# Kernel tuning notes

Hardware: AMD Instinct MI355X
Metric: run time of the kernel (lower is better)

The kernel has to match this reference:

```python
import jax, jax.numpy as jnp
import numpy as np

B, L, S, H, E, D = 2, 2048, 2048, 8, 64, 64

def setup_inputs() -> dict:
    key = jax.random.key(0)
    kq, kk, kv = jax.random.split(key, 3)
    queries = jax.random.normal(kq, (B, L, H, E), dtype=jnp.float32)
    keys = jax.random.normal(kk, (B, S, H, E), dtype=jnp.float32)
    values = jax.random.normal(kv, (B, S, H, D), dtype=jnp.float32)
    return {"queries": queries, "keys": keys, "values": values}

def reference(queries, keys, values):
    # queries: [B,L,H,E], keys: [B,S,H,E], values: [B,S,H,D]
    E_ = queries.shape[-1]
    scale = 1.0 / jnp.sqrt(jnp.asarray(E_, dtype=queries.dtype))
    # scores: [B,H,L,S]
    scores = jnp.einsum('blhe,bshe->bhls', queries, keys)
    # mask_flag=False, use_relative_pos=False, dropout=0.0 -> identity
    A = jax.nn.softmax(scale * scores, axis=-1)
    # output: [B,L,H,D]
    V = jnp.einsum('bhls,bshd->blhd', A, values)
    return V
```

## Files before the change

### kernel.cpp

```cpp
#include <hip/hip_runtime.h>
#include <hip/hip_bf16.h>


#define LOG2E 1.44269504088896340736f
#define SCL2 0.18033688011112042f

#if __has_builtin(__builtin_amdgcn_exp2f)
#define EXP2(x) __builtin_amdgcn_exp2f(x)
#else
#define EXP2(x) exp2f(x)
#endif

typedef __attribute__((ext_vector_type(8))) short bf16x8;
typedef __attribute__((ext_vector_type(4))) float f32x4;
typedef __attribute__((ext_vector_type(16))) float f32x16;

static constexpr int Bc = 2, Lc = 2048, Sc = 2048, Hc = 8, Ec = 64, Dc = 64;
static constexpr int BH = Bc * Hc;
static constexpr int ELEMS = Bc * Lc * Hc * Ec;

static __device__ __forceinline__ unsigned short bfb(float x) {
  union { __hip_bfloat16 h; unsigned short u; } c;
  c.h = __float2bfloat16(x);
  return c.u;
}
static __device__ __forceinline__ unsigned pkbf(float a, float b) {
  union { __hip_bfloat162 h; unsigned u; } c;
  c.h = __float22bfloat162_rn(make_float2(a, b));
  return c.u;
}
static __device__ __forceinline__ bf16x8 pack4(unsigned w0, unsigned w1,
                                               unsigned w2, unsigned w3) {
  union { unsigned u[4]; bf16x8 v; } c;
  c.u[0] = w0; c.u[1] = w1; c.u[2] = w2; c.u[3] = w3;
  return c.v;
}

static __device__ __forceinline__ void plswap(unsigned a, unsigned b,
                                              unsigned& o0, unsigned& o1, int hi) {
#if __has_builtin(__builtin_amdgcn_permlane32_swap)
  auto r = __builtin_amdgcn_permlane32_swap(a, b, false, false);
  o0 = r[0];
  o1 = r[1];
#else
  unsigned ax = (unsigned)__shfl_xor((int)a, 32);
  unsigned bx = (unsigned)__shfl_xor((int)b, 32);
  o0 = hi ? bx : a;
  o1 = hi ? b : ax;
#endif
}

__global__ __launch_bounds__(256) void prep_kv_kernel(const float* __restrict__ K,
                                                      const float* __restrict__ V,
                                                      __hip_bfloat16* __restrict__ Kc,
                                                      __hip_bfloat16* __restrict__ Vt) {
  __shared__ __hip_bfloat16 tile[4][64][68];
  if (blockIdx.x < 1024) {
    int t = blockIdx.x * 256 + threadIdx.x;
    int f = t * 8;
    int e = f & 63;
    int h = (f >> 6) & 7;
    int s = (f >> 9) & 2047;
    int b = f >> 20;
    float4 v0 = *reinterpret_cast<const float4*>(K + f);
    float4 v1 = *reinterpret_cast<const float4*>(K + f + 4);
    int es = e >> 4, hi = (e >> 3) & 1;
    int kb = s >> 5, qi = s & 31;
    int o = ((b << 3) + h) * (Sc * 64) + kb * 2048 + es * 512 + hi * 256 + qi * 8;
    union { ushort u[8]; uint4 q; } pk;
    pk.u[0] = bfb(v0.x); pk.u[1] = bfb(v0.y); pk.u[2] = bfb(v0.z); pk.u[3] = bfb(v0.w);
    pk.u[4] = bfb(v1.x); pk.u[5] = bfb(v1.y); pk.u[6] = bfb(v1.z); pk.u[7] = bfb(v1.w);
    *reinterpret_cast<uint4*>(Kc + o) = pk.q;
  } else {
    const int w = threadIdx.x >> 6;
    const int lane = threadIdx.x & 63;
    const int task = (blockIdx.x - 1024) * 4 + w;
    const int st = task & 31;
    const int bh = task >> 5;
    const int s0 = st * 64;
    const int b = bh >> 3, h = bh & 7;
#pragma unroll 4
    for (int j = 0; j < 64; ++j) {
      float v = V[((b * Sc + s0 + j) * Hc + h) * 64 + lane];
      tile[w][j][lane] = __float2bfloat16(v);
    }
    __syncthreads();
    const int qi = lane & 31, hi = lane >> 5;
    __hip_bfloat16* Vb = Vt + bh * (Sc * 64);
#pragma unroll
    for (int kb2 = 0; kb2 < 2; ++kb2)
#pragma unroll
      for (int d0 = 0; d0 < 2; ++d0)
#pragma unroll
        for (int ks = 0; ks < 2; ++ks) {
          union { ushort u[8]; uint4 q; } pk;
#pragma unroll
          for (int j = 0; j < 8; ++j) {
            union { __hip_bfloat16 h; ushort u; } c;
            c.h = tile[w][kb2 * 32 + ks * 16 + hi * 8 + j][d0 * 32 + qi];
            pk.u[j] = c.u;
          }
          int o = ((s0 >> 5) + kb2) * 2048 + d0 * 1024 + ks * 512 + lane * 8;
          *reinterpret_cast<uint4*>(Vb + o) = pk.q;
        }
  }
}

static __device__ __forceinline__ void sm_group(f32x16& sc, float& m, float& l,
                                                f32x16& oA, f32x16& oB, int hi,
                                                bf16x8& pb0, bf16x8& pb1) {
  float x0 = fmaxf(fmaxf(sc[0], sc[1]), fmaxf(sc[2], sc[3]));
  float x1 = fmaxf(fmaxf(sc[4], sc[5]), fmaxf(sc[6], sc[7]));
  float x2 = fmaxf(fmaxf(sc[8], sc[9]), fmaxf(sc[10], sc[11]));
  float x3 = fmaxf(fmaxf(sc[12], sc[13]), fmaxf(sc[14], sc[15]));
  float mx = fmaxf(fmaxf(x0, x1), fmaxf(x2, x3));
  unsigned ua, ub;
  plswap(__float_as_uint(mx), __float_as_uint(mx), ua, ub, hi);
  mx = fmaxf(__uint_as_float(ua), __uint_as_float(ub));

  if (__any(mx > m + 64.0f)) {
    float mnew = fmaxf(m, mx);
    float corr = EXP2((m - mnew) * SCL2);
    l *= corr;
#pragma unroll
    for (int r = 0; r < 16; ++r) { oA[r] *= corr; oB[r] *= corr; }
    m = mnew;
  }
  float mL = m * SCL2;
#pragma unroll
  for (int r = 0; r < 16; ++r) sc[r] = EXP2(sc[r] * SCL2 - mL);

  float r0 = (sc[0] + sc[1]) + (sc[2] + sc[3]);
  float r1 = (sc[4] + sc[5]) + (sc[6] + sc[7]);
  float r2 = (sc[8] + sc[9]) + (sc[10] + sc[11]);
  float r3 = (sc[12] + sc[13]) + (sc[14] + sc[15]);
  float rs = (r0 + r1) + (r2 + r3);
  plswap(__float_as_uint(rs), __float_as_uint(rs), ua, ub, hi);
  rs = __uint_as_float(ua) + __uint_as_float(ub);
  l += rs;

  unsigned c0, c1, c2, c3, y0, y1, y2, y3;
  c0 = pkbf(sc[0], sc[1]);  c1 = pkbf(sc[4], sc[5]);
  c2 = pkbf(sc[2], sc[3]);  c3 = pkbf(sc[6], sc[7]);
  plswap(c0, c1, y0, y2, hi);
  plswap(c2, c3, y1, y3, hi);
  pb0 = pack4(y0, y1, y2, y3);
  c0 = pkbf(sc[8], sc[9]);   c1 = pkbf(sc[12], sc[13]);
  c2 = pkbf(sc[10], sc[11]); c3 = pkbf(sc[14], sc[15]);
  plswap(c0, c1, y0, y2, hi);
  plswap(c2, c3, y1, y3, hi);
  pb1 = pack4(y0, y1, y2, y3);
}

__global__ __launch_bounds__(256, 2) void attn_kernel(const float* __restrict__ Qf,
                                                      const __hip_bfloat16* __restrict__ Kc,
                                                      const __hip_bfloat16* __restrict__ Vt,
                                                      float* __restrict__ Out) {
  __shared__ float obuf[4][2][16][64];
  __shared__ float mlb[2][4][2][32];

  const int lid = blockIdx.x;
  const int xcd = lid & 7;
  const int i = lid >> 3;
  const int bh = (xcd << 1) | (i >> 5);
  const int q0 = (i & 31) << 6;
  const int w = threadIdx.x >> 6;
  const int lane = threadIdx.x & 63;
  const int qi = lane & 31;
  const int hi = lane >> 5;
  const int b = bh >> 3, h = bh & 7;

  const __hip_bfloat16* Kh = Kc + bh * (Sc * 64);
  const __hip_bfloat16* Vh = Vt + bh * (Sc * 64);

  bf16x8 qf[2][4];
#pragma unroll
  for (int g = 0; g < 2; ++g) {
    const float* qrow = Qf + ((b * Lc + q0 + g * 32 + qi) * Hc + h) * 64 + hi * 8;
#pragma unroll
    for (int es = 0; es < 4; ++es) {
      float4 a = *reinterpret_cast<const float4*>(qrow + es * 16);
      float4 c = *reinterpret_cast<const float4*>(qrow + es * 16 + 4);
      qf[g][es] = pack4(pkbf(a.x, a.y), pkbf(a.z, a.w), pkbf(c.x, c.y), pkbf(c.z, c.w));
    }
  }

  f32x16 oa0, ob0, oa1, ob1;
#pragma unroll
  for (int r = 0; r < 16; ++r) { oa0[r] = 0.f; ob0[r] = 0.f; oa1[r] = 0.f; ob1[r] = 0.f; }
  float m0 = -1.0e30f, l0 = 0.f, m1 = -1.0e30f, l1 = 0.f;

  for (int s = w * 32; s < Sc; s += 128) {
    const __hip_bfloat16* Kp = Kh + (s >> 5) * 2048 + lane * 8;
    bf16x8 k0 = *reinterpret_cast<const bf16x8*>(Kp + 0 * 512);
    bf16x8 k1 = *reinterpret_cast<const bf16x8*>(Kp + 1 * 512);
    bf16x8 k2 = *reinterpret_cast<const bf16x8*>(Kp + 2 * 512);
    bf16x8 k3 = *reinterpret_cast<const bf16x8*>(Kp + 3 * 512);
    const __hip_bfloat16* Vp = Vh + (s >> 5) * 2048 + lane * 8;
    bf16x8 v00 = *reinterpret_cast<const bf16x8*>(Vp + 0 * 512);
    bf16x8 v01 = *reinterpret_cast<const bf16x8*>(Vp + 1 * 512);
    bf16x8 v10 = *reinterpret_cast<const bf16x8*>(Vp + 2 * 512);
    bf16x8 v11 = *reinterpret_cast<const bf16x8*>(Vp + 3 * 512);

    f32x16 sc0, sc1;
#pragma unroll
    for (int r = 0; r < 16; ++r) { sc0[r] = 0.f; sc1[r] = 0.f; }
    __builtin_amdgcn_s_setprio(1);
    sc0 = __builtin_amdgcn_mfma_f32_32x32x16_bf16(k0, qf[0][0], sc0, 0, 0, 0);
    sc0 = __builtin_amdgcn_mfma_f32_32x32x16_bf16(k1, qf[0][1], sc0, 0, 0, 0);
    sc0 = __builtin_amdgcn_mfma_f32_32x32x16_bf16(k2, qf[0][2], sc0, 0, 0, 0);
    sc0 = __builtin_amdgcn_mfma_f32_32x32x16_bf16(k3, qf[0][3], sc0, 0, 0, 0);
    sc1 = __builtin_amdgcn_mfma_f32_32x32x16_bf16(k0, qf[1][0], sc1, 0, 0, 0);
    sc1 = __builtin_amdgcn_mfma_f32_32x32x16_bf16(k1, qf[1][1], sc1, 0, 0, 0);
    sc1 = __builtin_amdgcn_mfma_f32_32x32x16_bf16(k2, qf[1][2], sc1, 0, 0, 0);
    sc1 = __builtin_amdgcn_mfma_f32_32x32x16_bf16(k3, qf[1][3], sc1, 0, 0, 0);
    __builtin_amdgcn_s_setprio(0);

    bf16x8 pb0, pb1;
    sm_group(sc0, m0, l0, oa0, ob0, hi, pb0, pb1);
    __builtin_amdgcn_s_setprio(1);
    oa0 = __builtin_amdgcn_mfma_f32_32x32x16_bf16(v00, pb0, oa0, 0, 0, 0);
    oa0 = __builtin_amdgcn_mfma_f32_32x32x16_bf16(v01, pb1, oa0, 0, 0, 0);
    ob0 = __builtin_amdgcn_mfma_f32_32x32x16_bf16(v10, pb0, ob0, 0, 0, 0);
    ob0 = __builtin_amdgcn_mfma_f32_32x32x16_bf16(v11, pb1, ob0, 0, 0, 0);
    __builtin_amdgcn_s_setprio(0);

    sm_group(sc1, m1, l1, oa1, ob1, hi, pb0, pb1);
    __builtin_amdgcn_s_setprio(1);
    oa1 = __builtin_amdgcn_mfma_f32_32x32x16_bf16(v00, pb0, oa1, 0, 0, 0);
    oa1 = __builtin_amdgcn_mfma_f32_32x32x16_bf16(v01, pb1, oa1, 0, 0, 0);
    ob1 = __builtin_amdgcn_mfma_f32_32x32x16_bf16(v10, pb0, ob1, 0, 0, 0);
    ob1 = __builtin_amdgcn_mfma_f32_32x32x16_bf16(v11, pb1, ob1, 0, 0, 0);
    __builtin_amdgcn_s_setprio(0);
  }

  if (hi == 0) {
    mlb[0][w][0][qi] = m0; mlb[0][w][1][qi] = l0;
    mlb[1][w][0][qi] = m1; mlb[1][w][1][qi] = l1;
  }
  __syncthreads();
  float myf[2], inv[2];
#pragma unroll
  for (int g = 0; g < 2; ++g) {
    float mm = fmaxf(fmaxf(mlb[g][0][0][qi], mlb[g][1][0][qi]),
                     fmaxf(mlb[g][2][0][qi], mlb[g][3][0][qi]));
    float Lt = 0.f;
#pragma unroll
    for (int sw = 0; sw < 4; ++sw)
      Lt += EXP2((mlb[g][sw][0][qi] - mm) * SCL2) * mlb[g][sw][1][qi];
    float mreg = g ? m1 : m0;
    myf[g] = EXP2((mreg - mm) * SCL2);
    inv[g] = 1.0f / Lt;
  }
  const int d0 = w >> 1, rr = (w & 1) * 8;
#pragma unroll
  for (int g = 0; g < 2; ++g) {
    if (g) __syncthreads();
    const f32x16& A = g ? oa1 : oa0;
    const f32x16& Bv = g ? ob1 : ob0;
#pragma unroll
    for (int r = 0; r < 16; ++r) {
      obuf[w][0][r][lane] = A[r] * myf[g];
      obuf[w][1][r][lane] = Bv[r] * myf[g];
    }
    __syncthreads();
    float* orow = Out + ((b * Lc + q0 + g * 32 + qi) * Hc + h) * Dc;
#pragma unroll
    for (int t = 0; t < 2; ++t) {
      f32x4 acc;
#pragma unroll
      for (int j = 0; j < 4; ++j) {
        const int r = rr + 4 * t + j;
        acc[j] = (obuf[0][d0][r][lane] + obuf[1][d0][r][lane] +
                  obuf[2][d0][r][lane] + obuf[3][d0][r][lane]) * inv[g];
      }
      const int dbase = d0 * 32 + ((rr + 4 * t) >> 2) * 8 + hi * 4;
      *reinterpret_cast<f32x4*>(orow + dbase) = acc;
    }
  }
}

extern "C" void kernel_launch(void* const* d_in, const int* in_sizes, int n_in,
                              void* d_out, int out_size, void* d_ws, size_t ws_size,
                              hipStream_t stream) {
  const float* Q = (const float*)d_in[0];
  const float* K = (const float*)d_in[1];
  const float* V = (const float*)d_in[2];
  float* out = (float*)d_out;

  __hip_bfloat16* Kc = (__hip_bfloat16*)d_ws;
  __hip_bfloat16* Vt = Kc + ELEMS;

  prep_kv_kernel<<<dim3(1152), 256, 0, stream>>>(K, V, Kc, Vt);
  attn_kernel<<<dim3(512), 256, 0, stream>>>(Q, Kc, Vt, out);
}
```

Before: 46.38 us.

## Double-buffer K/V register loads and defer cross-half softmax reductions

```diff
diff --git a/kernel.cpp b/kernel.cpp
--- a/kernel.cpp
+++ b/kernel.cpp
@@ -48,6 +48,16 @@
   o0 = hi ? bx : a;
   o1 = hi ? b : ax;
 #endif
+}
+static __device__ __forceinline__ float cross_half_max(float x, int hi) {
+  unsigned ua, ub;
+  plswap(__float_as_uint(x), __float_as_uint(x), ua, ub, hi);
+  return fmaxf(__uint_as_float(ua), __uint_as_float(ub));
+}
+static __device__ __forceinline__ float cross_half_sum(float x, int hi) {
+  unsigned ua, ub;
+  plswap(__float_as_uint(x), __float_as_uint(x), ua, ub, hi);
+  return __uint_as_float(ua) + __uint_as_float(ub);
 }
 
 __global__ __launch_bounds__(256) void prep_kv_kernel(const float* __restrict__ K,
@@ -114,12 +124,10 @@
   float x2 = fmaxf(fmaxf(sc[8], sc[9]), fmaxf(sc[10], sc[11]));
   float x3 = fmaxf(fmaxf(sc[12], sc[13]), fmaxf(sc[14], sc[15]));
   float mx = fmaxf(fmaxf(x0, x1), fmaxf(x2, x3));
-  unsigned ua, ub;
-  plswap(__float_as_uint(mx), __float_as_uint(mx), ua, ub, hi);
-  mx = fmaxf(__uint_as_float(ua), __uint_as_float(ub));
 
   if (__any(mx > m + 64.0f)) {
-    float mnew = fmaxf(m, mx);
+    float mrow = cross_half_max(mx, hi);
+    float mnew = fmaxf(m, mrow);
     float corr = EXP2((m - mnew) * SCL2);
     l *= corr;
 #pragma unroll
@@ -134,10 +142,7 @@
   float r1 = (sc[4] + sc[5]) + (sc[6] + sc[7]);
   float r2 = (sc[8] + sc[9]) + (sc[10] + sc[11]);
   float r3 = (sc[12] + sc[13]) + (sc[14] + sc[15]);
-  float rs = (r0 + r1) + (r2 + r3);
-  plswap(__float_as_uint(rs), __float_as_uint(rs), ua, ub, hi);
-  rs = __uint_as_float(ua) + __uint_as_float(ub);
-  l += rs;
+  l += (r0 + r1) + (r2 + r3);
 
   unsigned c0, c1, c2, c3, y0, y1, y2, y3;
   c0 = pkbf(sc[0], sc[1]);  c1 = pkbf(sc[4], sc[5]);
@@ -185,32 +190,39 @@
     }
   }
 
-  f32x16 oa0, ob0, oa1, ob1;
-#pragma unroll
-  for (int r = 0; r < 16; ++r) { oa0[r] = 0.f; ob0[r] = 0.f; oa1[r] = 0.f; ob1[r] = 0.f; }
+  f32x16 zero;
+#pragma unroll
+  for (int r = 0; r < 16; ++r) zero[r] = 0.f;
+
+  f32x16 oa0 = zero, ob0 = zero, oa1 = zero, ob1 = zero;
   float m0 = -1.0e30f, l0 = 0.f, m1 = -1.0e30f, l1 = 0.f;
 
-  for (int s = w * 32; s < Sc; s += 128) {
+  bf16x8 kA0, kA1, kA2, kA3, vA0, vA1, vA2, vA3;
+  bf16x8 kB0, kB1, kB2, kB3, vB0, vB1, vB2, vB3;
+
+  auto loadKV = [&](bf16x8& k0, bf16x8& k1, bf16x8& k2, bf16x8& k3,
+                    bf16x8& v0, bf16x8& v1, bf16x8& v2, bf16x8& v3, int s) {
     const __hip_bfloat16* Kp = Kh + (s >> 5) * 2048 + lane * 8;
-    bf16x8 k0 = *reinterpret_cast<const bf16x8*>(Kp + 0 * 512);
-    bf16x8 k1 = *reinterpret_cast<const bf16x8*>(Kp + 1 * 512);
-    bf16x8 k2 = *reinterpret_cast<const bf16x8*>(Kp + 2 * 512);
-    bf16x8 k3 = *reinterpret_cast<const bf16x8*>(Kp + 3 * 512);
+    k0 = *reinterpret_cast<const bf16x8*>(Kp + 0 * 512);
+    k1 = *reinterpret_cast<const bf16x8*>(Kp + 1 * 512);
+    k2 = *reinterpret_cast<const bf16x8*>(Kp + 2 * 512);
+    k3 = *reinterpret_cast<const bf16x8*>(Kp + 3 * 512);
     const __hip_bfloat16* Vp = Vh + (s >> 5) * 2048 + lane * 8;
-    bf16x8 v00 = *reinterpret_cast<const bf16x8*>(Vp + 0 * 512);
-    bf16x8 v01 = *reinterpret_cast<const bf16x8*>(Vp + 1 * 512);
-    bf16x8 v10 = *reinterpret_cast<const bf16x8*>(Vp + 2 * 512);
-    bf16x8 v11 = *reinterpret_cast<const bf16x8*>(Vp + 3 * 512);
-
+    v0 = *reinterpret_cast<const bf16x8*>(Vp + 0 * 512);
+    v1 = *reinterpret_cast<const bf16x8*>(Vp + 1 * 512);
+    v2 = *reinterpret_cast<const bf16x8*>(Vp + 2 * 512);
+    v3 = *reinterpret_cast<const bf16x8*>(Vp + 3 * 512);
+  };
+
+  auto compute = [&](bf16x8 k0, bf16x8 k1, bf16x8 k2, bf16x8 k3,
+                     bf16x8 v0, bf16x8 v1, bf16x8 v2, bf16x8 v3) {
     f32x16 sc0, sc1;
-#pragma unroll
-    for (int r = 0; r < 16; ++r) { sc0[r] = 0.f; sc1[r] = 0.f; }
     __builtin_amdgcn_s_setprio(1);
-    sc0 = __builtin_amdgcn_mfma_f32_32x32x16_bf16(k0, qf[0][0], sc0, 0, 0, 0);
+    sc0 = __builtin_amdgcn_mfma_f32_32x32x16_bf16(k0, qf[0][0], zero, 0, 0, 0);
     sc0 = __builtin_amdgcn_mfma_f32_32x32x16_bf16(k1, qf[0][1], sc0, 0, 0, 0);
     sc0 = __builtin_amdgcn_mfma_f32_32x32x16_bf16(k2, qf[0][2], sc0, 0, 0, 0);
     sc0 = __builtin_amdgcn_mfma_f32_32x32x16_bf16(k3, qf[0][3], sc0, 0, 0, 0);
-    sc1 = __builtin_amdgcn_mfma_f32_32x32x16_bf16(k0, qf[1][0], sc1, 0, 0, 0);
+    sc1 = __builtin_amdgcn_mfma_f32_32x32x16_bf16(k0, qf[1][0], zero, 0, 0, 0);
     sc1 = __builtin_amdgcn_mfma_f32_32x32x16_bf16(k1, qf[1][1], sc1, 0, 0, 0);
     sc1 = __builtin_amdgcn_mfma_f32_32x32x16_bf16(k2, qf[1][2], sc1, 0, 0, 0);
     sc1 = __builtin_amdgcn_mfma_f32_32x32x16_bf16(k3, qf[1][3], sc1, 0, 0, 0);
@@ -219,20 +231,32 @@
     bf16x8 pb0, pb1;
     sm_group(sc0, m0, l0, oa0, ob0, hi, pb0, pb1);
     __builtin_amdgcn_s_setprio(1);
-    oa0 = __builtin_amdgcn_mfma_f32_32x32x16_bf16(v00, pb0, oa0, 0, 0, 0);
-    oa0 = __builtin_amdgcn_mfma_f32_32x32x16_bf16(v01, pb1, oa0, 0, 0, 0);
-    ob0 = __builtin_amdgcn_mfma_f32_32x32x16_bf16(v10, pb0, ob0, 0, 0, 0);
-    ob0 = __builtin_amdgcn_mfma_f32_32x32x16_bf16(v11, pb1, ob0, 0, 0, 0);
+    oa0 = __builtin_amdgcn_mfma_f32_32x32x16_bf16(v0, pb0, oa0, 0, 0, 0);
+    oa0 = __builtin_amdgcn_mfma_f32_32x32x16_bf16(v1, pb1, oa0, 0, 0, 0);
+    ob0 = __builtin_amdgcn_mfma_f32_32x32x16_bf16(v2, pb0, ob0, 0, 0, 0);
+    ob0 = __builtin_amdgcn_mfma_f32_32x32x16_bf16(v3, pb1, ob0, 0, 0, 0);
     __builtin_amdgcn_s_setprio(0);
 
     sm_group(sc1, m1, l1, oa1, ob1, hi, pb0, pb1);
     __builtin_amdgcn_s_setprio(1);
-    oa1 = __builtin_amdgcn_mfma_f32_32x32x16_bf16(v00, pb0, oa1, 0, 0, 0);
-    oa1 = __builtin_amdgcn_mfma_f32_32x32x16_bf16(v01, pb1, oa1, 0, 0, 0);
-    ob1 = __builtin_amdgcn_mfma_f32_32x32x16_bf16(v10, pb0, ob1, 0, 0, 0);
-    ob1 = __builtin_amdgcn_mfma_f32_32x32x16_bf16(v11, pb1, ob1, 0, 0, 0);
+    oa1 = __builtin_amdgcn_mfma_f32_32x32x16_bf16(v0, pb0, oa1, 0, 0, 0);
+    oa1 = __builtin_amdgcn_mfma_f32_32x32x16_bf16(v1, pb1, oa1, 0, 0, 0);
+    ob1 = __builtin_amdgcn_mfma_f32_32x32x16_bf16(v2, pb0, ob1, 0, 0, 0);
+    ob1 = __builtin_amdgcn_mfma_f32_32x32x16_bf16(v3, pb1, ob1, 0, 0, 0);
     __builtin_amdgcn_s_setprio(0);
-  }
+  };
+
+  loadKV(kA0, kA1, kA2, kA3, vA0, vA1, vA2, vA3, w * 32);
+  for (int s = w * 32; s < Sc; s += 256) {
+    loadKV(kB0, kB1, kB2, kB3, vB0, vB1, vB2, vB3, s + 128);
+    compute(kA0, kA1, kA2, kA3, vA0, vA1, vA2, vA3);
+    if (s + 256 < Sc)
+      loadKV(kA0, kA1, kA2, kA3, vA0, vA1, vA2, vA3, s + 256);
+    compute(kB0, kB1, kB2, kB3, vB0, vB1, vB2, vB3);
+  }
+
+  l0 = cross_half_sum(l0, hi);
+  l1 = cross_half_sum(l1, hi);
 
   if (hi == 0) {
     mlb[0][w][0][qi] = m0; mlb[0][w][1][qi] = l0;
```

Measured after the change: 43.81 us. 1.06x faster.
